# Performance work log

Hardware: AMD Instinct MI355X
Metric: run time of the kernel (lower is better)

The kernel has to match this reference:

```python
import jax, jax.numpy as jnp
import numpy as np

N_HEADS = 16
N_KV_HEADS = 4
HEAD_DIM = 128  # d_model // n_heads = 2048 // 16
ROPE_THETA = 10000.0


def _rope_cos_sin(T, D, dtype):
    inv_freq = 1.0 / (ROPE_THETA ** (jnp.arange(0, D, 2, dtype=jnp.float32) / D))
    t = jnp.arange(T, dtype=jnp.float32)
    freqs = jnp.outer(t, inv_freq)               # [T, D/2]
    emb = jnp.concatenate([freqs, freqs], axis=-1)  # [T, D]
    return jnp.cos(emb).astype(dtype), jnp.sin(emb).astype(dtype)


def _rotate_half(x):
    x1, x2 = jnp.split(x, 2, axis=-1)
    return jnp.concatenate([-x2, x1], axis=-1)


def setup_inputs() -> dict:
    key = jax.random.key(0)
    k1, k2, k3, k4, k5 = jax.random.split(key, 5)
    B, T, C = 2, 2048, 2048
    H, KV, D = N_HEADS, N_KV_HEADS, HEAD_DIM
    s = 0.02
    return {
        "x": jax.random.normal(k1, (B, T, C), dtype=jnp.float32),
        "Wq": jax.random.normal(k2, (C, H * D), dtype=jnp.float32) * s,
        "Wk": jax.random.normal(k3, (C, KV * D), dtype=jnp.float32) * s,
        "Wv": jax.random.normal(k4, (C, KV * D), dtype=jnp.float32) * s,
        "Wo": jax.random.normal(k5, (H * D, C), dtype=jnp.float32) * s,
    }


def reference(x, Wq, Wk, Wv, Wo):
    B, T, C = x.shape
    H, KV, D = N_HEADS, N_KV_HEADS, HEAD_DIM
    G = H // KV
    scale = D ** -0.5

    q = (x @ Wq).reshape(B, T, H, D).transpose(0, 2, 1, 3)    # [B,H,T,D]
    k = (x @ Wk).reshape(B, T, KV, D).transpose(0, 2, 1, 3)   # [B,KV,T,D]
    v = (x @ Wv).reshape(B, T, KV, D).transpose(0, 2, 1, 3)   # [B,KV,T,D]

    cos, sin = _rope_cos_sin(T, D, x.dtype)  # [T,D] each, broadcasts over B,H
    q = q * cos + _rotate_half(q) * sin
    k = k * cos + _rotate_half(k) * sin

    # repeat_interleave kv heads to match query heads
    k = jnp.repeat(k, G, axis=1)  # [B,H,T,D]
    v = jnp.repeat(v, G, axis=1)  # [B,H,T,D]

    scores = jnp.einsum('bhqd,bhkd->bhqk', q, k) * scale  # [B,H,T,T]
    causal = jnp.tril(jnp.ones((T, T), dtype=bool))
    scores = jnp.where(causal, scores, jnp.finfo(scores.dtype).min)
    attn = jax.nn.softmax(scores, axis=-1)

    out = jnp.einsum('bhqk,bhkd->bhqd', attn, v)           # [B,H,T,D]
    out = out.transpose(0, 2, 1, 3).reshape(B, T, H * D)    # [B,T,C]
    return out @ Wo
```

## Files before the change

### kernel.cpp

```cpp
#include <hip/hip_runtime.h>
#include <cstdint>
#include <cstddef>

typedef __attribute__((ext_vector_type(4))) float f32x4;
typedef __attribute__((ext_vector_type(8))) short s16x8;
typedef __attribute__((ext_vector_type(4))) short s16x4;

#define B_  2
#define T_  2048
#define C_  2048
#define H_  16
#define KV_ 4
#define D_  128
#define M_  4096

static __device__ __forceinline__ float bf2f(ushort u){
  union { float f; uint32_t u; } x; x.u = ((uint32_t)u) << 16; return x.f;
}
static __device__ __forceinline__ ushort f2bf(float f){
  union { float f; uint32_t u; } x; x.f = f;
  uint32_t r = x.u + 0x7FFF + ((x.u >> 16) & 1);
  return (ushort)(r >> 16);
}

static __device__ __forceinline__ void gl_lds16(const ushort* g, ushort* s){
  __builtin_amdgcn_global_load_lds((const __attribute__((address_space(1))) void*)g,
                                   (__attribute__((address_space(3))) void*)s, 16, 0, 0);
}

__global__ void cvt_f32_bf16(const float* __restrict__ in, ushort* __restrict__ out, int n4){
  int idx = blockIdx.x * blockDim.x + threadIdx.x;
  int stride = gridDim.x * blockDim.x;
  for (int i = idx; i < n4; i += stride){
    float4 v = ((const float4*)in)[i];
    s16x4 o;
    o[0] = (short)f2bf(v.x); o[1] = (short)f2bf(v.y);
    o[2] = (short)f2bf(v.z); o[3] = (short)f2bf(v.w);
    ((s16x4*)out)[i] = o;
  }
}

__global__ void transpose_all(const float* __restrict__ Wq, const float* __restrict__ Wk,
                              const float* __restrict__ Wv, const float* __restrict__ Wo,
                              ushort* __restrict__ Wcat, ushort* __restrict__ Wot){
  __shared__ float tile[32][33];
  int bx = blockIdx.x;
  const float* W; ushort* Wt; int N; int n0; bool perm;
  if (bx < 64)      { W = Wq; Wt = Wcat;                          N = 2048; n0 = bx * 32;        perm = true;  }
  else if (bx < 80) { W = Wk; Wt = Wcat + (size_t)2048 * 2048;    N = 512;  n0 = (bx - 64) * 32; perm = true;  }
  else if (bx < 96) { W = Wv; Wt = Wcat + (size_t)2560 * 2048;    N = 512;  n0 = (bx - 80) * 32; perm = false; }
  else              { W = Wo; Wt = Wot;                           N = 2048; n0 = (bx - 96) * 32; perm = false; }
  int k0 = blockIdx.y * 32;
  int tx = threadIdx.x, ty = threadIdx.y;
  #pragma unroll
  for (int r = 0; r < 4; r++)
    tile[ty + 8*r][tx] = W[(size_t)(k0 + ty + 8*r) * N + n0 + tx];
  __syncthreads();
  #pragma unroll
  for (int r = 0; r < 4; r++){
    int nn = n0 + ty + 8*r;
    int dd = nn & 127;
    int dst_in = (((dd & 63) >> 4) << 5) | (((dd >> 6) & 1) << 4) | (dd & 15);
    int dst = perm ? ((nn & ~127) | dst_in) : nn;
    Wt[(size_t)dst * 2048 + k0 + tx] = f2bf(tile[tx][ty + 8*r]);
  }
}

template<int MODE>
__global__ __launch_bounds__(512)
void gemm_deep(const ushort* __restrict__ A, const ushort* __restrict__ Bt,
               void* __restrict__ C0, void* __restrict__ C1, void* __restrict__ C2,
               int N, int Kd, int nbx, float sq){
  __shared__ __align__(16) ushort Abuf[4][8192];
  __shared__ __align__(16) ushort Bbuf[4][8192];
  int tid = threadIdx.x, w = tid >> 6, l = tid & 63;
  int l15 = l & 15, l4 = l >> 4;

  int cpx = gridDim.x >> 3;
  int logical = (blockIdx.x & 7) * cpx + (blockIdx.x >> 3);
  int bx = logical % nbx, by = logical / nbx;
  int rblk = by * 128, cblk = bx * 128;
  int wm = w & 1, wn = w >> 1;

  int sr = tid >> 3;
  int sc = ((tid & 7) * 8) ^ ((sr & 7) << 3);
  const ushort* gA = A  + (size_t)(rblk + sr) * Kd + sc;
  const ushort* gB = Bt + (size_t)(cblk + sr) * Kd + sc;
  size_t rowK = (size_t)64 * Kd;
  int wb = w * 512;

  auto stage = [&](int t){
    int bsel = t & 3; int koff = t * 64;
    gl_lds16(gA + koff,        &Abuf[bsel][wb]);
    gl_lds16(gA + rowK + koff, &Abuf[bsel][4096 + wb]);
    gl_lds16(gB + koff,        &Bbuf[bsel][wb]);
    gl_lds16(gB + rowK + koff, &Bbuf[bsel][4096 + wb]);
  };

  int arow = wm * 64 + l15;
  int brow = wn * 32 + l15;
  int kx0 = (l4 * 8) ^ ((l15 & 7) << 3);
  int kx1 = (32 + l4 * 8) ^ ((l15 & 7) << 3);

  f32x4 acc[4][2] = {};

  auto phase = [&](int t, int dostage, int vm){
    const ushort* Ab = Abuf[t & 3];
    const ushort* Bb = Bbuf[t & 3];
    s16x8 a[4][2], b[2][2];
    #pragma unroll
    for (int m = 0; m < 4; m++){
      a[m][0] = *(const s16x8*)(Ab + (arow + m*16) * 64 + kx0);
      a[m][1] = *(const s16x8*)(Ab + (arow + m*16) * 64 + kx1);
    }
    #pragma unroll
    for (int n = 0; n < 2; n++){
      b[n][0] = *(const s16x8*)(Bb + (brow + n*16) * 64 + kx0);
      b[n][1] = *(const s16x8*)(Bb + (brow + n*16) * 64 + kx1);
    }
    if (dostage) stage(t + 3);
    if (vm == 8)      { asm volatile("s_waitcnt vmcnt(8)" ::: "memory"); }
    else if (vm == 4) { asm volatile("s_waitcnt vmcnt(4)" ::: "memory"); }
    else if (vm == 0) { asm volatile("s_waitcnt vmcnt(0)" ::: "memory"); }
    asm volatile("s_waitcnt lgkmcnt(0)" ::: "memory");
    __builtin_amdgcn_sched_barrier(0);
    __builtin_amdgcn_s_barrier();
    __builtin_amdgcn_s_setprio(1);
    #pragma unroll
    for (int m = 0; m < 4; m++)
      #pragma unroll
      for (int n = 0; n < 2; n++){
        acc[m][n] = __builtin_amdgcn_mfma_f32_16x16x32_bf16(a[m][0], b[n][0], acc[m][n], 0, 0, 0);
        acc[m][n] = __builtin_amdgcn_mfma_f32_16x16x32_bf16(a[m][1], b[n][1], acc[m][n], 0, 0, 0);
      }
    __builtin_amdgcn_s_setprio(0);
  };

  stage(0); stage(1); stage(2);
  asm volatile("s_waitcnt vmcnt(8)" ::: "memory");
  __builtin_amdgcn_s_barrier();

  int nt = Kd >> 6;
  #pragma unroll 1
  for (int t = 0; t < nt - 3; ++t) phase(t, 1, 8);
  phase(nt - 3, 0, 4);
  phase(nt - 2, 0, 0);
  phase(nt - 1, 0, -1);

  if (MODE == 0){
    #pragma unroll
    for (int m = 0; m < 4; m++)
      #pragma unroll
      for (int n = 0; n < 2; n++)
        #pragma unroll
        for (int j = 0; j < 4; j++){
          int row = rblk + wm*64 + m*16 + l4*4 + j;
          int col = cblk + wn*32 + n*16 + l15;
          ((float*)C0)[(size_t)row * N + col] = acc[m][n][j];
        }
  } else if (cblk < 2560){
    float scale = (cblk < 2048) ? sq : 1.0f;
    int hh = (cblk < 2048) ? (cblk >> 7) : ((cblk - 2048) >> 7);
    int nh = (cblk < 2048) ? H_ : KV_;
    ushort* base = (ushort*)((cblk < 2048) ? C0 : C1);
    int i = wn * 16 + l15;
    float invf = exp2f(-(float)i * 0.2076205059304602f);
    #pragma unroll
    for (int m = 0; m < 4; m++){
      #pragma unroll
      for (int j = 0; j < 4; j++){
        int row = rblk + wm*64 + m*16 + l4*4 + j;
        int t = row & (T_ - 1), bb = row >> 11;
        float s, co;
        __sincosf((float)t * invf, &s, &co);
        float v0 = acc[m][0][j], v1 = acc[m][1][j];
        size_t roff = (((size_t)(bb * nh + hh)) * T_ + t) * D_;
        base[roff + i]      = f2bf((v0 * co - v1 * s) * scale);
        base[roff + i + 64] = f2bf((v1 * co + v0 * s) * scale);
      }
    }
  } else {
    #pragma unroll
    for (int m = 0; m < 4; m++)
      #pragma unroll
      for (int n = 0; n < 2; n++)
        #pragma unroll
        for (int j = 0; j < 4; j++){
          int row = rblk + wm*64 + m*16 + l4*4 + j;
          int col = cblk + wn*32 + n*16 + l15;
          int t = row & (T_ - 1), bb = row >> 11;
          int c2 = col - 2560;
          int hh = c2 >> 7, d = c2 & 127;
          ((ushort*)C2)[(((size_t)(bb * KV_ + hh)) * D_ + d) * T_ + t] = f2bf(acc[m][n][j]);
        }
  }
}

__global__ __launch_bounds__(512, 4)
void attn_kernel7(const ushort* __restrict__ Q, const ushort* __restrict__ Kc,
                  const ushort* __restrict__ Vt, ushort* __restrict__ O){
  __shared__ __align__(16) ushort Ks[2][64 * 128];
  __shared__ __align__(16) ushort Vs[2][128 * 64];
  __shared__ __align__(16) ushort Ps[8 * 16 * 64];
  int bid = blockIdx.x;
  int i  = bid >> 3;
  int qt = (i < 32) ? (63 - i) : (i - 32);
  int sub = bid & 7;
  int b = sub >> 2, kvh = sub & 3;
  int tid = threadIdx.x, w = tid >> 6, l = tid & 63;
  int l15 = l & 15, l4 = l >> 4;
  int sw3 = (l15 & 7) << 3;
  int q0 = qt * 32;
  int hq = kvh * 4 + (w >> 1);
  int qrow0 = q0 + (w & 1) * 16;
  int qrow = qrow0 + l15;

  s16x8 qf[4];
  const ushort* qbase = Q + (((size_t)(b * H_ + hq)) * T_ + qrow) * D_;
  #pragma unroll
  for (int kk = 0; kk < 4; kk++)
    qf[kk] = *(const s16x8*)(qbase + kk * 32 + l4 * 8);

  f32x4 oacc[8] = {};
  float mrun = -1e30f;
  float rsum = 0.f;
  const float THR = 11.5415603f;
  ushort* Pw = Ps + w * (16 * 64) + l15 * 64;

  const ushort* kbase = Kc + ((size_t)(b * KV_ + kvh)) * T_ * D_;
  const ushort* vbase = Vt + ((size_t)(b * KV_ + kvh)) * D_ * T_;
  int jmax = (q0 + 31) >> 6;

  int kr0 = tid >> 4, kcb = tid & 15;
  int vd0 = tid >> 3, vtb = tid & 7;
  int ksoff = kr0 * 128 + ((kcb * 8) ^ ((kr0 & 7) << 3));
  int vsoff = vd0 * 64  + ((vtb * 8) ^ ((vd0 & 7) << 3));
  const ushort* kg = kbase + (size_t)kr0 * D_ + kcb * 8;
  const ushort* vg = vbase + (size_t)vd0 * T_ + vtb * 8;

  s16x8 kreg0, kreg1, vreg0, vreg1;
  kreg0 = *(const s16x8*)(kg);
  kreg1 = *(const s16x8*)(kg + (size_t)32 * D_);
  vreg0 = *(const s16x8*)(vg);
  vreg1 = *(const s16x8*)(vg + (size_t)64 * T_);

  for (int jt = 0; jt <= jmax; jt++){
    ushort* Ksc = Ks[jt & 1];
    ushort* Vsc = Vs[jt & 1];
    *(s16x8*)(Ksc + ksoff)            = kreg0;
    *(s16x8*)(Ksc + ksoff + 32 * 128) = kreg1;
    *(s16x8*)(Vsc + vsoff)            = vreg0;
    *(s16x8*)(Vsc + vsoff + 64 * 64)  = vreg1;
    __syncthreads();
    if (jt < jmax){
      int k1 = (jt + 1) * 64;
      kreg0 = *(const s16x8*)(kg + (size_t)k1 * D_);
      kreg1 = *(const s16x8*)(kg + (size_t)(k1 + 32) * D_);
      vreg0 = *(const s16x8*)(vg + k1);
      vreg1 = *(const s16x8*)(vg + (size_t)64 * T_ + k1);
    }
    int k0 = jt * 64;

    f32x4 sacc[4] = {};
    __builtin_amdgcn_s_setprio(1);
    #pragma unroll
    for (int kk = 0; kk < 4; kk++){
      #pragma unroll
      for (int n = 0; n < 4; n++){
        s16x8 kf = *(const s16x8*)(Ksc + (16*n + l15) * 128 + ((kk*32 + l4*8) ^ sw3));
        sacc[n] = __builtin_amdgcn_mfma_f32_16x16x32_bf16(kf, qf[kk], sacc[n], 0, 0, 0);
      }
    }
    __builtin_amdgcn_s_setprio(0);
    if (jt == jmax){
      #pragma unroll
      for (int n = 0; n < 4; n++)
        #pragma unroll
        for (int j = 0; j < 4; j++){
          int kcol = k0 + 16*n + 4*l4 + j;
          if (kcol > qrow) sacc[n][j] = -1e30f;
        }
    }
    float mloc = -1e30f;
    #pragma unroll
    for (int n = 0; n < 4; n++)
      #pragma unroll
      for (int j = 0; j < 4; j++)
        mloc = fmaxf(mloc, sacc[n][j]);
    if (__any((int)(mloc > mrun + THR))){
      float m2 = fmaxf(mloc, __shfl_xor(mloc, 16));
      m2 = fmaxf(m2, __shfl_xor(m2, 32));
      float mnew = fmaxf(mrun, m2);
      float alpha = exp2f(mrun - mnew);
      mrun = mnew;
      rsum *= alpha;
      #pragma unroll
      for (int n8 = 0; n8 < 8; n8++)
        #pragma unroll
        for (int j = 0; j < 4; j++)
          oacc[n8][j] *= alpha;
    }
    #pragma unroll
    for (int n = 0; n < 4; n++){
      float p0 = exp2f(sacc[n][0] - mrun);
      float p1 = exp2f(sacc[n][1] - mrun);
      float p2 = exp2f(sacc[n][2] - mrun);
      float p3 = exp2f(sacc[n][3] - mrun);
      rsum += (p0 + p1) + (p2 + p3);
      uint32_t lo, hi;
      asm volatile("v_cvt_pk_bf16_f32 %0, %1, %2" : "=v"(lo) : "v"(p0), "v"(p1));
      asm volatile("v_cvt_pk_bf16_f32 %0, %1, %2" : "=v"(hi) : "v"(p2), "v"(p3));
      uint2 pk; pk.x = lo; pk.y = hi;
      *(uint2*)(Pw + ((16*n + 4*l4) ^ sw3)) = pk;
    }
    __builtin_amdgcn_s_setprio(1);
    #pragma unroll
    for (int kk = 0; kk < 2; kk++){
      s16x8 pf = *(const s16x8*)(Pw + ((kk*32 + l4*8) ^ sw3));
      #pragma unroll
      for (int n8 = 0; n8 < 8; n8++){
        s16x8 vf = *(const s16x8*)(Vsc + (16*n8 + l15) * 64 + ((kk*32 + l4*8) ^ sw3));
        oacc[n8] = __builtin_amdgcn_mfma_f32_16x16x32_bf16(vf, pf, oacc[n8], 0, 0, 0);
      }
    }
    __builtin_amdgcn_s_setprio(0);
  }

  rsum += __shfl_xor(rsum, 16);
  rsum += __shfl_xor(rsum, 32);
  float inv = 1.f / rsum;
  ushort* obase = O + ((size_t)(b * T_ + qrow)) * C_ + hq * D_ + 4*l4;
  #pragma unroll
  for (int n8 = 0; n8 < 8; n8++){
    s16x4 ov;
    #pragma unroll
    for (int j = 0; j < 4; j++)
      ov[j] = (short)f2bf(oacc[n8][j] * inv);
    *(s16x4*)(obase + 16*n8) = ov;
  }
}

extern "C" void kernel_launch(void* const* d_in, const int* in_sizes, int n_in,
                              void* d_out, int out_size, void* d_ws, size_t ws_size,
                              hipStream_t stream){
  const float* x  = (const float*)d_in[0];
  const float* Wq = (const float*)d_in[1];
  const float* Wk = (const float*)d_in[2];
  const float* Wv = (const float*)d_in[3];
  const float* Wo = (const float*)d_in[4];
  float* out = (float*)d_out;

  char* ws = (char*)d_ws;
  size_t off = 0;
  auto alloc = [&](size_t bytes)->void*{
    void* p = ws + off; off += (bytes + 255) & ~(size_t)255; return p;
  };
  ushort* xb   = (ushort*)alloc((size_t)M_ * C_ * 2);
  ushort* Wcat = (ushort*)alloc((size_t)3072 * 2048 * 2);
  ushort* Wot  = (ushort*)alloc((size_t)2048 * 2048 * 2);
  ushort* Qb   = (ushort*)alloc((size_t)B_ * H_ * T_ * D_ * 2);
  ushort* Kb   = (ushort*)alloc((size_t)B_ * KV_ * T_ * D_ * 2);
  ushort* Vtb  = (ushort*)alloc((size_t)B_ * KV_ * T_ * D_ * 2);
  ushort* Ob   = (ushort*)alloc((size_t)M_ * C_ * 2);

  cvt_f32_bf16<<<2048, 256, 0, stream>>>(x, xb, M_ * C_ / 4);
  transpose_all<<<dim3(160, 64), dim3(32, 8), 0, stream>>>(Wq, Wk, Wv, Wo, Wcat, Wot);

  gemm_deep<1><<<768, 512, 0, stream>>>(xb, Wcat, Qb, Kb, Vtb, 3072, 2048, 24,
                                        0.08838834764831845f * 1.4426950408889634f);

  attn_kernel7<<<512, 512, 0, stream>>>(Qb, Kb, Vtb, Ob);

  gemm_deep<0><<<512, 512, 0, stream>>>(Ob, Wot, out, nullptr, nullptr, 2048, 2048, 16, 0.f);
}
```

Baseline: 184.2 us.

## Software-pipeline attention: overlap next QK^T with current softmax and PV

Restructures the attention loop so the QK^T MFMA for tile t runs before the softmax and PV of tile t-1. K/V shared buffers go from double to triple buffering so the previous tile's V stays resident. The causal mask moves to a peeled final iteration. Launch bounds drop from 4 to 1 blocks per SM, which frees registers for the extra live score accumulators but may reduce occupancy and latency hiding.

```diff
diff --git a/kernel.cpp b/kernel.cpp
--- a/kernel.cpp
+++ b/kernel.cpp
@@ -196,11 +196,11 @@
   }
 }
 
-__global__ __launch_bounds__(512, 4)
-void attn_kernel7(const ushort* __restrict__ Q, const ushort* __restrict__ Kc,
+__global__ __launch_bounds__(512, 1)
+void attn_kernel8(const ushort* __restrict__ Q, const ushort* __restrict__ Kc,
                   const ushort* __restrict__ Vt, ushort* __restrict__ O){
-  __shared__ __align__(16) ushort Ks[2][64 * 128];
-  __shared__ __align__(16) ushort Vs[2][128 * 64];
+  __shared__ __align__(16) ushort Ks[3][64 * 128];
+  __shared__ __align__(16) ushort Vs[3][128 * 64];
   __shared__ __align__(16) ushort Ps[8 * 16 * 64];
   int bid = blockIdx.x;
   int i  = bid >> 3;
@@ -244,24 +244,8 @@
   vreg0 = *(const s16x8*)(vg);
   vreg1 = *(const s16x8*)(vg + (size_t)64 * T_);
 
-  for (int jt = 0; jt <= jmax; jt++){
-    ushort* Ksc = Ks[jt & 1];
-    ushort* Vsc = Vs[jt & 1];
-    *(s16x8*)(Ksc + ksoff)            = kreg0;
-    *(s16x8*)(Ksc + ksoff + 32 * 128) = kreg1;
-    *(s16x8*)(Vsc + vsoff)            = vreg0;
-    *(s16x8*)(Vsc + vsoff + 64 * 64)  = vreg1;
-    __syncthreads();
-    if (jt < jmax){
-      int k1 = (jt + 1) * 64;
-      kreg0 = *(const s16x8*)(kg + (size_t)k1 * D_);
-      kreg1 = *(const s16x8*)(kg + (size_t)(k1 + 32) * D_);
-      vreg0 = *(const s16x8*)(vg + k1);
-      vreg1 = *(const s16x8*)(vg + (size_t)64 * T_ + k1);
-    }
-    int k0 = jt * 64;
-
-    f32x4 sacc[4] = {};
+  auto qk = [&](int sel, f32x4 (&sacc)[4]){
+    const ushort* Ksc = Ks[sel];
     __builtin_amdgcn_s_setprio(1);
     #pragma unroll
     for (int kk = 0; kk < 4; kk++){
@@ -272,15 +256,10 @@
       }
     }
     __builtin_amdgcn_s_setprio(0);
-    if (jt == jmax){
-      #pragma unroll
-      for (int n = 0; n < 4; n++)
-        #pragma unroll
-        for (int j = 0; j < 4; j++){
-          int kcol = k0 + 16*n + 4*l4 + j;
-          if (kcol > qrow) sacc[n][j] = -1e30f;
-        }
-    }
+  };
+
+  auto smpv = [&](f32x4 (&sacc)[4], int vsel){
+    const ushort* Vsc = Vs[vsel];
     float mloc = -1e30f;
     #pragma unroll
     for (int n = 0; n < 4; n++)
@@ -324,6 +303,58 @@
       }
     }
     __builtin_amdgcn_s_setprio(0);
+  };
+
+  {
+    ushort* Ksc = Ks[0]; ushort* Vsc = Vs[0];
+    *(s16x8*)(Ksc + ksoff)            = kreg0;
+    *(s16x8*)(Ksc + ksoff + 32 * 128) = kreg1;
+    *(s16x8*)(Vsc + vsoff)            = vreg0;
+    *(s16x8*)(Vsc + vsoff + 64 * 64)  = vreg1;
+    __syncthreads();
+  }
+  f32x4 sp[4] = {};
+  qk(0, sp);
+  if (jmax > 0){
+    kreg0 = *(const s16x8*)(kg + (size_t)64 * D_);
+    kreg1 = *(const s16x8*)(kg + (size_t)96 * D_);
+    vreg0 = *(const s16x8*)(vg + 64);
+    vreg1 = *(const s16x8*)(vg + (size_t)64 * T_ + 64);
+  }
+
+  #pragma unroll 1
+  for (int t = 1; t <= jmax; ++t){
+    int sel = t % 3;
+    ushort* Ksc = Ks[sel]; ushort* Vsc = Vs[sel];
+    *(s16x8*)(Ksc + ksoff)            = kreg0;
+    *(s16x8*)(Ksc + ksoff + 32 * 128) = kreg1;
+    *(s16x8*)(Vsc + vsoff)            = vreg0;
+    *(s16x8*)(Vsc + vsoff + 64 * 64)  = vreg1;
+    __syncthreads();
+    f32x4 scur[4] = {};
+    qk(sel, scur);
+    smpv(sp, (t - 1) % 3);
+    if (t < jmax){
+      int k1 = (t + 1) * 64;
+      kreg0 = *(const s16x8*)(kg + (size_t)k1 * D_);
+      kreg1 = *(const s16x8*)(kg + (size_t)(k1 + 32) * D_);
+      vreg0 = *(const s16x8*)(vg + k1);
+      vreg1 = *(const s16x8*)(vg + (size_t)64 * T_ + k1);
+    }
+    #pragma unroll
+    for (int n = 0; n < 4; n++) sp[n] = scur[n];
+  }
+
+  {
+    int k0 = jmax * 64;
+    #pragma unroll
+    for (int n = 0; n < 4; n++)
+      #pragma unroll
+      for (int j = 0; j < 4; j++){
+        int kcol = k0 + 16*n + 4*l4 + j;
+        if (kcol > qrow) sp[n][j] = -1e30f;
+      }
+    smpv(sp, jmax % 3);
   }
 
   rsum += __shfl_xor(rsum, 16);
@@ -369,7 +400,7 @@
   gemm_deep<1><<<768, 512, 0, stream>>>(xb, Wcat, Qb, Kb, Vtb, 3072, 2048, 24,
                                         0.08838834764831845f * 1.4426950408889634f);
 
-  attn_kernel7<<<512, 512, 0, stream>>>(Qb, Kb, Vtb, Ob);
+  attn_kernel8<<<512, 512, 0, stream>>>(Qb, Kb, Vtb, Ob);
 
   gemm_deep<0><<<512, 512, 0, stream>>>(Ob, Wot, out, nullptr, nullptr, 2048, 2048, 16, 0.f);
 }
```

After: 199.0 us. 8.1% more time.
